# Performance work log

Hardware: AMD Instinct MI355X
Metric: run time of the kernel (lower is better)

Reference implementation:

```python
import jax, jax.numpy as jnp
import numpy as np

B, N, K, L, H = 8, 2048, 16, 4, 8
CONV = (64, 64, 128, 256)
W_DIM, N_CODES, E_DIM, P_DIM, FF = 512, 8, 64, 256, 512


def act(x):
    return jax.nn.leaky_relu(x, 0.2)


def ln(x, g, b, eps=1e-5):
    m = jnp.mean(x, -1, keepdims=True)
    v = jnp.mean((x - m) ** 2, -1, keepdims=True)
    return g * (x - m) / jnp.sqrt(v + eps) + b


# per-batch neighbor gather: f [C,N], i [N,K] -> [C,N,K]
gather_nb = jax.vmap(lambda f, i: f[:, i])


def knn_idx(y):  # y [B,3,N] -> [B,N,K]
    xx = jnp.sum(y * y, axis=1)
    inner = jnp.einsum('bcn,bcm->bnm', y, y)
    dist = 2.0 * inner - xx[:, :, None] - xx[:, None, :]  # negative sq dist
    return jax.lax.top_k(dist, K)[1]


def mha(q, kv, Wq, bq, Wk, bk, Wv, bv, Wo, bo):
    Bq, S, D = q.shape
    Sk = kv.shape[1]
    dh = D // H
    qh = (q @ Wq.T + bq).reshape(Bq, S, H, dh)
    kh = (kv @ Wk.T + bk).reshape(Bq, Sk, H, dh)
    vh = (kv @ Wv.T + bv).reshape(Bq, Sk, H, dh)
    a = jax.nn.softmax(jnp.einsum('bqhd,bkhd->bhqk', qh, kh) * (1.0 / np.sqrt(dh)))
    o = jnp.einsum('bhqk,bkhd->bqhd', a, vh).reshape(Bq, S, D)
    return o @ Wo.T + bo


def setup_inputs() -> dict:
    key = jax.random.key(0)
    ks = iter(jax.random.split(key, 48))
    nrm = lambda shape: jax.random.normal(next(ks), shape, jnp.float32) * 0.02
    d = {
        'x': jax.random.normal(next(ks), (B, N, 3), jnp.float32),
        'W_ec': nrm((CONV[0], 6)), 'b_ec': jnp.zeros((CONV[0],), jnp.float32),
        'Wc1': nrm((CONV[1], CONV[0])), 'bc1': jnp.zeros((CONV[1],), jnp.float32),
        'Wc2': nrm((CONV[2], CONV[1])), 'bc2': jnp.zeros((CONV[2],), jnp.float32),
        'Wc3': nrm((CONV[3], CONV[2])), 'bc3': jnp.zeros((CONV[3],), jnp.float32),
        'Wf': nrm((W_DIM, sum(CONV))), 'bf': jnp.zeros((W_DIM,), jnp.float32),
        'Wpc': nrm((P_DIM, E_DIM)), 'bpc': jnp.zeros((P_DIM,), jnp.float32),
        'Wpi': nrm((P_DIM, 3)), 'bpi': jnp.zeros((P_DIM,), jnp.float32),
        'Wq': nrm((L, 2, P_DIM, P_DIM)), 'bq': jnp.zeros((L, 2, P_DIM), jnp.float32),
        'Wk': nrm((L, 2, P_DIM, P_DIM)), 'bk': jnp.zeros((L, 2, P_DIM), jnp.float32),
        'Wv': nrm((L, 2, P_DIM, P_DIM)), 'bv': jnp.zeros((L, 2, P_DIM), jnp.float32),
        'Wo': nrm((L, 2, P_DIM, P_DIM)), 'bo': jnp.zeros((L, 2, P_DIM), jnp.float32),
        'ln1g': jnp.ones((L, P_DIM), jnp.float32), 'ln1b': jnp.zeros((L, P_DIM), jnp.float32),
        'ln2g': jnp.ones((L, P_DIM), jnp.float32), 'ln2b': jnp.zeros((L, P_DIM), jnp.float32),
        'Wff1': nrm((L, FF, P_DIM)), 'bff1': jnp.zeros((L, FF), jnp.float32),
        'Wff2': nrm((L, P_DIM, FF)), 'bff2': jnp.zeros((L, P_DIM), jnp.float32),
        'ln3g': jnp.ones((L, P_DIM), jnp.float32), 'ln3b': jnp.zeros((L, P_DIM), jnp.float32),
        'lnfg': jnp.ones((P_DIM,), jnp.float32), 'lnfb': jnp.zeros((P_DIM,), jnp.float32),
        'Wcm': nrm((E_DIM, P_DIM)), 'bcm': jnp.zeros((E_DIM,), jnp.float32),
    }
    return d


def reference(x, W_ec, b_ec, Wc1, bc1, Wc2, bc2, Wc3, bc3, Wf, bf, Wpc, bpc, Wpi, bpi,
              Wq, bq, Wk, bk, Wv, bv, Wo, bo, ln1g, ln1b, ln2g, ln2b,
              Wff1, bff1, Wff2, bff2, ln3g, ln3b, lnfg, lnfb, Wcm, bcm):
    y = jnp.transpose(x, (0, 2, 1))                      # [B,3,N]
    idx = knn_idx(y)                                     # [B,N,K]
    nb = gather_nb(y, idx)                               # [B,3,N,K]
    feats = jnp.concatenate([nb - y[..., None], jnp.broadcast_to(y[..., None], nb.shape)], axis=1)
    h = act(jnp.einsum('oc,bcnk->bonk', W_ec, feats) + b_ec[:, None, None])
    h = h.max(axis=3)                                    # [B,64,N]
    xs = [h]
    for Wl, bl in ((Wc1, bc1), (Wc2, bc2), (Wc3, bc3)):
        h = gather_nb(h, idx).max(axis=3)                # graph max pooling
        h = act(jnp.einsum('oc,bcn->bon', Wl, h) + bl[:, None])
        xs.append(h)
    h = jnp.concatenate(xs, axis=1)                      # [B,512,N]
    h = jnp.einsum('oc,bcn->bon', Wf, h) + bf[:, None]
    xm = h.max(axis=2)                                   # [B,512]
    q = act(xm.reshape(B, N_CODES, E_DIM) @ Wpc.T + bpc) # [B,8,256]
    mem = act(x @ Wpi.T + bpi)                           # [B,N,256]
    for l in range(L):
        q = ln(q + mha(q, q, Wq[l, 0], bq[l, 0], Wk[l, 0], bk[l, 0], Wv[l, 0], bv[l, 0], Wo[l, 0], bo[l, 0]), ln1g[l], ln1b[l])
        q = ln(q + mha(q, mem, Wq[l, 1], bq[l, 1], Wk[l, 1], bk[l, 1], Wv[l, 1], bv[l, 1], Wo[l, 1], bo[l, 1]), ln2g[l], ln2b[l])
        q = ln(q + (act(q @ Wff1[l].T + bff1[l]) @ Wff2[l].T + bff2[l]), ln3g[l], ln3b[l])
    q = ln(q, lnfg, lnfb)
    out = q @ Wcm.T + bcm                                # [B,8,64]
    return out.reshape(B, W_DIM)
```

## Files before the change

### kernel.cpp

```cpp
#include <hip/hip_runtime.h>
#include <math.h>

#define BN 8
#define NP 2048
#define KNN 16
#define NL 4
#define NH 8

typedef __attribute__((ext_vector_type(8))) short bf16x8;
typedef __attribute__((ext_vector_type(4))) float f32x4;

__device__ __forceinline__ unsigned short f2bf(float f) {
    unsigned u = __float_as_uint(f);
    unsigned r = (u + 0x7FFFu + ((u >> 16) & 1u)) >> 16;
    return (unsigned short)r;
}
__device__ __forceinline__ float bf2f(unsigned short s) {
    return __uint_as_float(((unsigned)s) << 16);
}
__device__ __forceinline__ unsigned fmono(float f) {
    unsigned u = __float_as_uint(f);
    return (u & 0x80000000u) ? ~u : (u | 0x80000000u);
}
__device__ __forceinline__ float funmono(unsigned k) {
    return (k & 0x80000000u) ? __uint_as_float(k ^ 0x80000000u) : __uint_as_float(~k);
}

__device__ __forceinline__ float gemv_dot(const unsigned short* __restrict__ wrow, const float* sm, int K8) {
    const uint4* w8 = (const uint4*)wrow;
    const float4* r4 = (const float4*)sm;
    float acc = 0.f;
    #pragma unroll 16
    for (int c = 0; c < K8; ++c) {
        uint4 wv = w8[c];
        float4 a0 = r4[c * 2], a1 = r4[c * 2 + 1];
        acc += a0.x * __uint_as_float(wv.x << 16);
        acc += a0.y * __uint_as_float(wv.x & 0xFFFF0000u);
        acc += a0.z * __uint_as_float(wv.y << 16);
        acc += a0.w * __uint_as_float(wv.y & 0xFFFF0000u);
        acc += a1.x * __uint_as_float(wv.z << 16);
        acc += a1.y * __uint_as_float(wv.z & 0xFFFF0000u);
        acc += a1.z * __uint_as_float(wv.w << 16);
        acc += a1.w * __uint_as_float(wv.w & 0xFFFF0000u);
    }
    return acc;
}

__device__ __forceinline__ unsigned long long shflx_u64(unsigned long long v, int j) {
    int lo = __shfl_xor((int)(unsigned)(v & 0xFFFFFFFFull), j);
    int hi = __shfl_xor((int)(unsigned)(v >> 32), j);
    return ((unsigned long long)(unsigned)hi << 32) | (unsigned)lo;
}

__device__ __forceinline__ unsigned sort64_u32(unsigned v, int lane) {
    #pragma unroll
    for (int k = 2; k <= 64; k <<= 1) {
        #pragma unroll
        for (int j = k >> 1; j > 0; j >>= 1) {
            unsigned o = (unsigned)__shfl_xor((int)v, j);
            bool up = ((lane & k) == 0);
            bool lower = ((lane & j) == 0);
            unsigned mn = v < o ? v : o;
            unsigned mx = v < o ? o : v;
            v = (up == lower) ? mn : mx;
        }
    }
    return v;
}

__device__ __forceinline__ unsigned long long sort64_u64(unsigned long long v, int lane) {
    #pragma unroll
    for (int k = 2; k <= 64; k <<= 1) {
        #pragma unroll
        for (int j = k >> 1; j > 0; j >>= 1) {
            unsigned long long o = shflx_u64(v, j);
            bool up = ((lane & k) == 0);
            bool lower = ((lane & j) == 0);
            unsigned long long mn = v < o ? v : o;
            unsigned long long mx = v < o ? o : v;
            v = (up == lower) ? mn : mx;
        }
    }
    return v;
}

__global__ __launch_bounds__(256) void knn_kernel(const float* __restrict__ x, int* __restrict__ idxout) {
    __shared__ unsigned long long cand[4][64];
    int tid = threadIdx.x;
    int wv = tid >> 6, lane = tid & 63;
    int p = blockIdx.x * 4 + wv;
    int b = p >> 11, n = p & 2047;
    const float* xb = x + (size_t)b * NP * 3;
    float cx = xb[n * 3 + 0], cy = xb[n * 3 + 1], cz = xb[n * 3 + 2];
    float xn = cx * cx + cy * cy + cz * cz;
    unsigned key[32];
    unsigned lmax = 0u;
    #pragma unroll
    for (int t = 0; t < 32; ++t) {
        int m = (t << 6) | lane;
        float mx = xb[m * 3 + 0], my = xb[m * 3 + 1], mz = xb[m * 3 + 2];
        float xxm = mx * mx + my * my + mz * mz;
        float inner = cx * mx + cy * my + cz * mz;
        float dd = 2.0f * inner - xn - xxm;
        unsigned u = __float_as_uint(dd);
        u = (u & 0x80000000u) ? ~u : (u | 0x80000000u);
        key[t] = u;
        lmax = lmax > u ? lmax : u;
    }
    unsigned sorted = sort64_u32(lmax, lane);
    unsigned S = (unsigned)__shfl((int)sorted, 48);
    int c = 0;
    #pragma unroll
    for (int t = 0; t < 32; ++t) c += (key[t] >= S) ? 1 : 0;
    int inc = c;
    #pragma unroll
    for (int d = 1; d < 64; d <<= 1) {
        int tsh = __shfl_up(inc, d);
        if (lane >= d) inc += tsh;
    }
    int C = __shfl(inc, 63);
    int* op = idxout + (size_t)p * KNN;
    if (C <= 64) {
        int off = inc - c;
        #pragma unroll
        for (int t = 0; t < 32; ++t) {
            if (key[t] >= S) {
                int m = (t << 6) | lane;
                cand[wv][off++] = ((unsigned long long)key[t] << 16) | (unsigned)(2047 - m);
            }
        }
        asm volatile("s_waitcnt lgkmcnt(0)" ::: "memory");
        unsigned long long ck = (lane < C) ? cand[wv][lane] : 0ull;
        ck = sort64_u64(ck, lane);
        if (lane >= 48) op[63 - lane] = 2047 - (int)(unsigned)(ck & 0xFFFFull);
    } else {
        unsigned taken = 0u;
        for (int r = 0; r < KNN; ++r) {
            unsigned long long best = 0ull;
            #pragma unroll
            for (int t = 0; t < 32; ++t) {
                if (!((taken >> t) & 1u)) {
                    int m = (t << 6) | lane;
                    unsigned long long ck = ((unsigned long long)key[t] << 16) | (unsigned)(2047 - m);
                    if (ck > best) best = ck;
                }
            }
            #pragma unroll
            for (int d = 1; d < 64; d <<= 1) {
                unsigned long long o = shflx_u64(best, d);
                if (o > best) best = o;
            }
            int m = 2047 - (int)(unsigned)(best & 0xFFFFull);
            if (lane == 0) op[r] = m;
            if ((m & 63) == lane) taken |= 1u << (m >> 6);
        }
    }
}

__global__ __launch_bounds__(256) void edge_conv_kernel(const float* __restrict__ x, const int* __restrict__ idx,
                                                        const float* __restrict__ Wec, const float* __restrict__ bec,
                                                        unsigned short* __restrict__ hcatT) {
    int tid = threadIdx.x;
    int g = tid >> 6, o = tid & 63;
    int p = blockIdx.x * 4 + g;
    int b = p >> 11;
    __shared__ float nb[4][KNN][3];
    __shared__ float ctr[4][3];
    if (o < KNN) {
        int j = idx[(size_t)p * KNN + o];
        const float* xp = x + ((size_t)b * NP + j) * 3;
        nb[g][o][0] = xp[0]; nb[g][o][1] = xp[1]; nb[g][o][2] = xp[2];
    }
    if (o >= KNN && o < KNN + 3) ctr[g][o - KNN] = x[(size_t)p * 3 + (o - KNN)];
    __syncthreads();
    float w0 = Wec[o * 6 + 0], w1 = Wec[o * 6 + 1], w2 = Wec[o * 6 + 2];
    float w3 = Wec[o * 6 + 3], w4 = Wec[o * 6 + 4], w5 = Wec[o * 6 + 5];
    float c0 = ctr[g][0], c1 = ctr[g][1], c2 = ctr[g][2];
    float base = bec[o] + w3 * c0 + w4 * c1 + w5 * c2;
    float m = -3.4e38f;
    #pragma unroll
    for (int k = 0; k < KNN; ++k) {
        float v = base + w0 * (nb[g][k][0] - c0) + w1 * (nb[g][k][1] - c1) + w2 * (nb[g][k][2] - c2);
        v = v > 0.f ? v : 0.2f * v;
        m = fmaxf(m, v);
    }
    hcatT[(size_t)p * 512 + o] = f2bf(m);
}

__global__ __launch_bounds__(256) void pool_bf16_kernel(const unsigned short* __restrict__ src, int s_coff,
                                                        const int* __restrict__ idx,
                                                        unsigned short* __restrict__ dst, int C) {
    int tid = threadIdx.x, wv = tid >> 6, lane = tid & 63;
    int p = blockIdx.x * 4 + wv;
    int b = p >> 11;
    const int* ip = idx + (size_t)p * KNN;
    const unsigned short* sb = src + (size_t)b * NP * 512 + s_coff;
    for (int c0 = 0; c0 < C; c0 += 64) {
        int ch = c0 + lane;
        float m = -3.4e38f;
        #pragma unroll
        for (int k = 0; k < KNN; ++k) {
            int j = ip[k];
            m = fmaxf(m, bf2f(sb[(size_t)j * 512 + ch]));
        }
        dst[(size_t)p * C + ch] = f2bf(m);
    }
}

__global__ __launch_bounds__(256) void mfma_conv64_kernel(const unsigned short* __restrict__ A,
                                                          const unsigned short* __restrict__ W,
                                                          const float* __restrict__ bias,
                                                          unsigned short* __restrict__ hcatT, int coff) {
    __shared__ unsigned short As[128][72];
    __shared__ unsigned short Bs[64][72];
    int m0 = blockIdx.x * 128, b = blockIdx.z;
    int tid = threadIdx.x;
    int lane = tid & 63, wave = tid >> 6;
    int wr = wave >> 1, wc = wave & 1;
    int quad = lane >> 4, l16 = lane & 15;
    {
        int r = tid >> 1, s = (tid & 1) * 32;
        const unsigned short* ap = A + (size_t)b * NP * 64 + (size_t)(m0 + r) * 64 + s;
        uint4 v0 = *(const uint4*)(ap);
        uint4 v1 = *(const uint4*)(ap + 8);
        uint4 v2 = *(const uint4*)(ap + 16);
        uint4 v3 = *(const uint4*)(ap + 24);
        *(uint4*)&As[r][s] = v0; *(uint4*)&As[r][s + 8] = v1;
        *(uint4*)&As[r][s + 16] = v2; *(uint4*)&As[r][s + 24] = v3;
    }
    {
        int r = tid >> 2, s = (tid & 3) * 16;
        const unsigned short* wp = W + r * 64 + s;
        *(uint4*)&Bs[r][s] = *(const uint4*)wp;
        *(uint4*)&Bs[r][s + 8] = *(const uint4*)(wp + 8);
    }
    __syncthreads();
    f32x4 acc[4][2] = {};
    #pragma unroll
    for (int k0 = 0; k0 < 64; k0 += 32) {
        bf16x8 af[4], bfv[2];
        #pragma unroll
        for (int i = 0; i < 4; ++i) af[i] = *(const bf16x8*)&As[wr * 64 + i * 16 + l16][k0 + quad * 8];
        #pragma unroll
        for (int j = 0; j < 2; ++j) bfv[j] = *(const bf16x8*)&Bs[wc * 32 + j * 16 + l16][k0 + quad * 8];
        #pragma unroll
        for (int i = 0; i < 4; ++i)
            #pragma unroll
            for (int j = 0; j < 2; ++j)
                acc[i][j] = __builtin_amdgcn_mfma_f32_16x16x32_bf16(af[i], bfv[j], acc[i][j], 0, 0, 0);
    }
    #pragma unroll
    for (int i = 0; i < 4; ++i) {
        #pragma unroll
        for (int r = 0; r < 4; ++r) {
            int pt = m0 + wr * 64 + i * 16 + quad * 4 + r;
            #pragma unroll
            for (int j = 0; j < 2; ++j) {
                int ch = wc * 32 + j * 16 + l16;
                float v = acc[i][j][r] + bias[ch];
                v = v > 0.f ? v : 0.2f * v;
                hcatT[((size_t)b * NP + pt) * 512 + coff + ch] = f2bf(v);
            }
        }
    }
}

__global__ __launch_bounds__(256) void wcast_kernel(const float* __restrict__ Wf, const float* __restrict__ Wc3,
                                                    const float* __restrict__ Wk, const float* __restrict__ Wv,
                                                    const float* __restrict__ bk, const float* __restrict__ bv,
                                                    const float* __restrict__ Wc1, const float* __restrict__ Wc2,
                                                    const float* __restrict__ Wq, const float* __restrict__ Wo,
                                                    const float* __restrict__ Wff1, const float* __restrict__ Wff2,
                                                    unsigned short* __restrict__ WfB, unsigned short* __restrict__ Wc3B,
                                                    unsigned short* __restrict__ WkvB, float* __restrict__ bkv,
                                                    unsigned short* __restrict__ Wc1B, unsigned short* __restrict__ Wc2B,
                                                    unsigned short* __restrict__ WtB, unsigned short* __restrict__ Wff1B,
                                                    unsigned short* __restrict__ Wff2B,
                                                    unsigned* __restrict__ xmk) {
    int id = blockIdx.x * 256 + threadIdx.x;
    if (id < 262144) { WfB[id] = f2bf(Wf[id]); return; }
    int j = id - 262144;
    if (j < 32768) { Wc3B[j] = f2bf(Wc3[j]); return; }
    j -= 32768;
    if (j < 524288) {
        int l = j >> 17, r = j & 131071;
        float v = (r < 65536) ? Wk[(size_t)(l * 2 + 1) * 65536 + r]
                              : Wv[(size_t)(l * 2 + 1) * 65536 + (r - 65536)];
        WkvB[j] = f2bf(v);
        return;
    }
    j -= 524288;
    if (j < 2048) {
        int l = j >> 9, r = j & 511;
        bkv[j] = (r < 256) ? bk[(l * 2 + 1) * 256 + r] : bv[(l * 2 + 1) * 256 + (r - 256)];
        return;
    }
    j -= 2048;
    if (j < 4096) { Wc1B[j] = f2bf(Wc1[j]); return; }
    j -= 4096;
    if (j < 8192) { Wc2B[j] = f2bf(Wc2[j]); return; }
    j -= 8192;
    if (j < 4096) { xmk[j] = 0u; return; }
    j -= 4096;
    if (j < 1572864) {
        int l = j / 393216;
        int r = j - l * 393216;
        int m = r >> 16, c = r & 65535;
        float v;
        if (m == 0)      v = Wq[(size_t)(l * 2 + 0) * 65536 + c];
        else if (m == 1) v = Wk[(size_t)(l * 2 + 0) * 65536 + c];
        else if (m == 2) v = Wv[(size_t)(l * 2 + 0) * 65536 + c];
        else if (m == 3) v = Wo[(size_t)(l * 2 + 0) * 65536 + c];
        else if (m == 4) v = Wq[(size_t)(l * 2 + 1) * 65536 + c];
        else             v = Wo[(size_t)(l * 2 + 1) * 65536 + c];
        WtB[j] = f2bf(v);
        return;
    }
    j -= 1572864;
    if (j < 524288) { Wff1B[j] = f2bf(Wff1[j]); return; }
    j -= 524288;
    if (j < 524288) { Wff2B[j] = f2bf(Wff2[j]); return; }
}

__global__ __launch_bounds__(256) void mfma_gemm_kernel(const unsigned short* __restrict__ A, size_t a_bstride,
                                                        const unsigned short* __restrict__ B, size_t b_bstride,
                                                        const float* __restrict__ bias, int bias_per_m,
                                                        void* __restrict__ C, size_t c_bstride, int c_rstride,
                                                        int K, int act, int out_bf16,
                                                        unsigned* __restrict__ xmk, int domax) {
    __shared__ unsigned short As[128][40];
    __shared__ unsigned short Bs[128][40];
    int m0 = blockIdx.x * 128, n0 = blockIdx.y * 128, b = blockIdx.z;
    int tid = threadIdx.x;
    int lane = tid & 63, wave = tid >> 6;
    int wr = wave >> 1, wc = wave & 1;
    int quad = lane >> 4, l16 = lane & 15;
    int r0 = tid >> 2, kc0 = (tid & 3) * 8;
    f32x4 acc[4][4] = {};
    const unsigned short* Ab = A + (size_t)b * a_bstride;
    const unsigned short* Bb = B + (size_t)b * b_bstride;
    for (int k0 = 0; k0 < K; k0 += 32) {
        uint4 a0 = *(const uint4*)(Ab + (size_t)(m0 + r0) * K + k0 + kc0);
        uint4 a1 = *(const uint4*)(Ab + (size_t)(m0 + r0 + 64) * K + k0 + kc0);
        uint4 b0 = *(const uint4*)(Bb + (size_t)(n0 + r0) * K + k0 + kc0);
        uint4 b1 = *(const uint4*)(Bb + (size_t)(n0 + r0 + 64) * K + k0 + kc0);
        __syncthreads();
        *(uint4*)&As[r0][kc0] = a0;
        *(uint4*)&As[r0 + 64][kc0] = a1;
        *(uint4*)&Bs[r0][kc0] = b0;
        *(uint4*)&Bs[r0 + 64][kc0] = b1;
        __syncthreads();
        bf16x8 af[4], bfv[4];
        #pragma unroll
        for (int i = 0; i < 4; ++i) af[i] = *(const bf16x8*)&As[wr * 64 + i * 16 + l16][quad * 8];
        #pragma unroll
        for (int j = 0; j < 4; ++j) bfv[j] = *(const bf16x8*)&Bs[wc * 64 + j * 16 + l16][quad * 8];
        #pragma unroll
        for (int i = 0; i < 4; ++i)
            #pragma unroll
            for (int j = 0; j < 4; ++j)
                acc[i][j] = __builtin_amdgcn_mfma_f32_16x16x32_bf16(af[i], bfv[j], acc[i][j], 0, 0, 0);
    }
    if (domax) {
        #pragma unroll
        for (int i = 0; i < 4; ++i) {
            #pragma unroll
            for (int r = 0; r < 4; ++r) {
                int m = m0 + wr * 64 + i * 16 + quad * 4 + r;
                float v = fmaxf(fmaxf(acc[i][0][r], acc[i][1][r]), fmaxf(acc[i][2][r], acc[i][3][r]));
                v += bias[m];
                #pragma unroll
                for (int off = 1; off <= 8; off <<= 1) v = fmaxf(v, __shfl_xor(v, off));
                if (l16 == 0) atomicMax(&xmk[(size_t)b * 512 + m], fmono(v));
            }
        }
        return;
    }
    #pragma unroll
    for (int i = 0; i < 4; ++i) {
        #pragma unroll
        for (int r = 0; r < 4; ++r) {
            int m = m0 + wr * 64 + i * 16 + quad * 4 + r;
            float bm = bias_per_m ? bias[m] : 0.f;
            #pragma unroll
            for (int j = 0; j < 4; ++j) {
                int n = n0 + wc * 64 + j * 16 + l16;
                float v = acc[i][j][r] + (bias_per_m ? bm : bias[n]);
                if (act) v = v > 0.f ? v : 0.2f * v;
                size_t off = (size_t)b * c_bstride + (size_t)m * c_rstride + n;
                if (out_bf16) ((unsigned short*)C)[off] = f2bf(v);
                else          ((float*)C)[off] = v;
            }
        }
    }
}

__global__ __launch_bounds__(256) void mfma_kv_all_kernel(const unsigned short* __restrict__ A,
                                                          const unsigned short* __restrict__ W,
                                                          const float* __restrict__ bkv,
                                                          unsigned short* __restrict__ KVall) {
    __shared__ unsigned short As[128][40];
    __shared__ unsigned short Bs[128][40];
    int m0 = blockIdx.x * 128;
    int nb = blockIdx.y & 3, l = blockIdx.y >> 2;
    int n0 = nb * 128;
    int b = blockIdx.z;
    int tid = threadIdx.x;
    int lane = tid & 63, wave = tid >> 6;
    int wr = wave >> 1, wc = wave & 1;
    int quad = lane >> 4, l16 = lane & 15;
    int r0 = tid >> 2, kc0 = (tid & 3) * 8;
    f32x4 acc[4][4] = {};
    const unsigned short* Ab = A + (size_t)b * NP * 256;
    const unsigned short* Bb = W + (size_t)l * 131072;
    const float* bias = bkv + l * 512;
    for (int k0 = 0; k0 < 256; k0 += 32) {
        uint4 a0 = *(const uint4*)(Ab + (size_t)(m0 + r0) * 256 + k0 + kc0);
        uint4 a1 = *(const uint4*)(Ab + (size_t)(m0 + r0 + 64) * 256 + k0 + kc0);
        uint4 b0 = *(const uint4*)(Bb + (size_t)(n0 + r0) * 256 + k0 + kc0);
        uint4 b1 = *(const uint4*)(Bb + (size_t)(n0 + r0 + 64) * 256 + k0 + kc0);
        __syncthreads();
        *(uint4*)&As[r0][kc0] = a0;
        *(uint4*)&As[r0 + 64][kc0] = a1;
        *(uint4*)&Bs[r0][kc0] = b0;
        *(uint4*)&Bs[r0 + 64][kc0] = b1;
        __syncthreads();
        bf16x8 af[4], bfv[4];
        #pragma unroll
        for (int i = 0; i < 4; ++i) af[i] = *(const bf16x8*)&As[wr * 64 + i * 16 + l16][quad * 8];
        #pragma unroll
        for (int j = 0; j < 4; ++j) bfv[j] = *(const bf16x8*)&Bs[wc * 64 + j * 16 + l16][quad * 8];
        #pragma unroll
        for (int i = 0; i < 4; ++i)
            #pragma unroll
            for (int j = 0; j < 4; ++j)
                acc[i][j] = __builtin_amdgcn_mfma_f32_16x16x32_bf16(af[i], bfv[j], acc[i][j], 0, 0, 0);
    }
    unsigned short* Cb = KVall + ((size_t)l * BN + b) * NP * 512;
    #pragma unroll
    for (int i = 0; i < 4; ++i) {
        #pragma unroll
        for (int r = 0; r < 4; ++r) {
            int m = m0 + wr * 64 + i * 16 + quad * 4 + r;
            #pragma unroll
            for (int j = 0; j < 4; ++j) {
                int n = n0 + wc * 64 + j * 16 + l16;
                Cb[(size_t)m * 512 + n] = f2bf(acc[i][j][r] + bias[n]);
            }
        }
    }
}

__global__ __launch_bounds__(256) void pc_kernel(const unsigned* __restrict__ xmk, const float* __restrict__ Wpc,
                                                 const float* __restrict__ bpc, float* __restrict__ q) {
    int id = blockIdx.x * 256 + threadIdx.x;
    int p = id & 255;
    int rowi = id >> 8;
    int b = rowi >> 3, i = rowi & 7;
    const unsigned* xr = xmk + b * 512 + i * 64;
    const float* w = Wpc + (size_t)p * 64;
    float acc = bpc[p];
    #pragma unroll
    for (int e = 0; e < 64; ++e) acc += funmono(xr[e]) * w[e];
    q[id] = acc > 0.f ? acc : 0.2f * acc;
}

__global__ __launch_bounds__(256) void mem_kernel(const float* __restrict__ x, const float* __restrict__ Wpi,
                                                  const float* __restrict__ bpi, unsigned short* __restrict__ memB) {
    size_t id = (size_t)blockIdx.x * 256 + threadIdx.x;
    int p = (int)(id & 255);
    size_t pt = id >> 8;
    float x0 = x[pt * 3 + 0], x1 = x[pt * 3 + 1], x2 = x[pt * 3 + 2];
    float v = bpi[p] + x0 * Wpi[p * 3 + 0] + x1 * Wpi[p * 3 + 1] + x2 * Wpi[p * 3 + 2];
    v = v > 0.f ? v : 0.2f * v;
    memB[id] = f2bf(v);
}

__global__ __launch_bounds__(256) void qkv_proj_kernel(const float* __restrict__ in,
                                                       const unsigned short* __restrict__ WB,
                                                       const float* __restrict__ bq0, const float* __restrict__ bk0,
                                                       const float* __restrict__ bv0,
                                                       float* __restrict__ Qs, float* __restrict__ Ks,
                                                       float* __restrict__ Vs) {
    int which = blockIdx.y;
    const unsigned short* W = WB + (size_t)which * 65536;
    const float* bb = (which == 0) ? bq0 : (which == 1) ? bk0 : bv0;
    float* out = (which == 0) ? Qs : (which == 1) ? Ks : Vs;
    __shared__ __align__(16) float r[256];
    int row = blockIdx.x, tid = threadIdx.x;
    r[tid] = in[(size_t)row * 256 + tid];
    __syncthreads();
    float acc = bb[tid] + gemv_dot(W + (size_t)tid * 256, r, 32);
    out[(size_t)row * 256 + tid] = acc;
}

__global__ __launch_bounds__(256) void attn_ln_kernel(const float* __restrict__ Qs, const float* __restrict__ Ks,
                                                      const float* __restrict__ Vs,
                                                      const unsigned short* __restrict__ WoB,
                                                      const float* __restrict__ bo, const float* __restrict__ res,
                                                      const float* __restrict__ g, const float* __restrict__ bt,
                                                      const unsigned short* __restrict__ Wq1B,
                                                      const float* __restrict__ bq1,
                                                      float* __restrict__ out, float* __restrict__ Qc) {
    int row = blockIdx.x, tid = threadIdx.x;
    int b = row >> 3;
    __shared__ float Kl[2048], Vl[2048], qr[256];
    __shared__ float sc[64];
    __shared__ __align__(16) float r[256];
    __shared__ __align__(16) float aout[256];
    __shared__ float red[256];
    for (int t = tid; t < 2048; t += 256) {
        Kl[t] = Ks[(size_t)b * 2048 + t];
        Vl[t] = Vs[(size_t)b * 2048 + t];
    }
    qr[tid] = Qs[(size_t)row * 256 + tid];
    __syncthreads();
    const float scale = 0.17677669529663687f;
    if (tid < 64) {
        int h = tid >> 3, k = tid & 7;
        float dot = 0.f;
        #pragma unroll
        for (int d = 0; d < 32; ++d) dot += qr[h * 32 + d] * Kl[k * 256 + h * 32 + d];
        sc[tid] = dot * scale;
    }
    __syncthreads();
    if (tid < 8) {
        float* p = sc + tid * 8;
        float m = -3.4e38f;
        #pragma unroll
        for (int k = 0; k < 8; ++k) m = fmaxf(m, p[k]);
        float s = 0.f;
        #pragma unroll
        for (int k = 0; k < 8; ++k) { p[k] = __expf(p[k] - m); s += p[k]; }
        float inv = 1.f / s;
        #pragma unroll
        for (int k = 0; k < 8; ++k) p[k] *= inv;
    }
    __syncthreads();
    {
        int h = tid >> 5;
        float acc = 0.f;
        #pragma unroll
        for (int k = 0; k < 8; ++k) acc += sc[h * 8 + k] * Vl[k * 256 + tid];
        r[tid] = acc;
    }
    __syncthreads();
    float acc = bo[tid] + gemv_dot(WoB + (size_t)tid * 256, r, 32);
    float v = res[(size_t)row * 256 + tid] + acc;
    red[tid] = v; __syncthreads();
    for (int s = 128; s; s >>= 1) { if (tid < s) red[tid] += red[tid + s]; __syncthreads(); }
    float mean = red[0] * (1.0f / 256.0f);
    __syncthreads();
    float dv = v - mean;
    red[tid] = dv * dv; __syncthreads();
    for (int s = 128; s; s >>= 1) { if (tid < s) red[tid] += red[tid + s]; __syncthreads(); }
    float var = red[0] * (1.0f / 256.0f);
    float oln = g[tid] * dv * rsqrtf(var + 1e-5f) + bt[tid];
    out[(size_t)row * 256 + tid] = oln;
    aout[tid] = oln;
    __syncthreads();
    {
        float qacc = bq1[tid] + gemv_dot(Wq1B + (size_t)tid * 256, aout, 32);
        Qc[(size_t)row * 256 + tid] = qacc;
    }
}

__global__ __launch_bounds__(256) void ca_part_kernel(const float* __restrict__ Qc,
                                                      const unsigned short* __restrict__ KVl,
                                                      float* __restrict__ part) {
    int kb = blockIdx.x, h = blockIdx.y, b = blockIdx.z;
    int tid = threadIdx.x;
    __shared__ float q[8][32];
    __shared__ __align__(16) float S[8][128];
    __shared__ float om[8][8][32];
    const float scale = 0.17677669529663687f;
    {
        int i = tid >> 5, d = tid & 31;
        q[i][d] = Qc[(size_t)(b * 8 + i) * 256 + h * 32 + d];
    }
    __syncthreads();
    {
        int kk = tid & 127, half = tid >> 7;
        int k = kb * 128 + kk;
        const unsigned short* kp = KVl + ((size_t)b * NP + k) * 512 + h * 32;
        float kd[32];
        #pragma unroll
        for (int u = 0; u < 4; ++u) {
            uint4 raw = *(const uint4*)(kp + u * 8);
            unsigned w0 = raw.x, w1 = raw.y, w2 = raw.z, w3 = raw.w;
            kd[u * 8 + 0] = __uint_as_float(w0 << 16); kd[u * 8 + 1] = __uint_as_float(w0 & 0xFFFF0000u);
            kd[u * 8 + 2] = __uint_as_float(w1 << 16); kd[u * 8 + 3] = __uint_as_float(w1 & 0xFFFF0000u);
            kd[u * 8 + 4] = __uint_as_float(w2 << 16); kd[u * 8 + 5] = __uint_as_float(w2 & 0xFFFF0000u);
            kd[u * 8 + 6] = __uint_as_float(w3 << 16); kd[u * 8 + 7] = __uint_as_float(w3 & 0xFFFF0000u);
        }
        #pragma unroll
        for (int i = 0; i < 4; ++i) {
            int ri = half * 4 + i;
            float dot = 0.f;
            #pragma unroll
            for (int d = 0; d < 32; ++d) dot += q[ri][d] * kd[d];
            S[ri][kk] = dot * scale;
        }
    }
    __syncthreads();
    float* pout = part + (((size_t)(b * NH + h)) * 16 + kb) * 288;
    {
        int i = tid >> 5, l32 = tid & 31;
        float m = -3.4e38f;
        #pragma unroll
        for (int t = 0; t < 4; ++t) m = fmaxf(m, S[i][l32 + t * 32]);
        #pragma unroll
        for (int off = 16; off; off >>= 1) m = fmaxf(m, __shfl_xor(m, off));
        float s = 0.f;
        #pragma unroll
        for (int t = 0; t < 4; ++t) {
            float e = __expf(S[i][l32 + t * 32] - m);
            S[i][l32 + t * 32] = e;
            s += e;
        }
        #pragma unroll
        for (int off = 16; off; off >>= 1) s += __shfl_xor(s, off);
        if (l32 == 0) { pout[i] = m; pout[8 + i] = s; }
    }
    __syncthreads();
    {
        int d = tid & 31, grp = tid >> 5;
        const unsigned short* Vb = KVl + ((size_t)b * NP + kb * 128) * 512 + 256 + h * 32 + d;
        float acc[8] = {};
        #pragma unroll 4
        for (int t = 0; t < 16; ++t) {
            int kk = grp * 16 + t;
            float v = bf2f(Vb[(size_t)kk * 512]);
            #pragma unroll
            for (int i = 0; i < 8; ++i) acc[i] += S[i][kk] * v;
        }
        #pragma unroll
        for (int i = 0; i < 8; ++i) om[grp][i][d] = acc[i];
    }
    __syncthreads();
    {
        int i = tid >> 5, d = tid & 31;
        float sum = 0.f;
        #pragma unroll
        for (int g = 0; g < 8; ++g) sum += om[g][i][d];
        pout[16 + i * 32 + d] = sum;
    }
}

__global__ __launch_bounds__(256) void combine_ff_kernel(const float* __restrict__ part,
                                                         const unsigned short* __restrict__ WoB,
                                                         const float* __restrict__ bo, const float* __restrict__ res,
                                                         const float* __restrict__ g2, const float* __restrict__ b2t,
                                                         const unsigned short* __restrict__ W1B,
                                                         const float* __restrict__ b1,
                                                         const unsigned short* __restrict__ W2B,
                                                         const float* __restrict__ b2,
                                                         const float* __restrict__ g3, const float* __restrict__ b3t,
                                                         float* __restrict__ out,
                                                         int is_last, const float* __restrict__ lnfg,
                                                         const float* __restrict__ lnfb, const float* __restrict__ Wcm,
                                                         const float* __restrict__ bcm, float* __restrict__ finout) {
    int row = blockIdx.x, tid = threadIdx.x;
    int b = row >> 3, i = row & 7;
    __shared__ __align__(16) float r[256];
    __shared__ __align__(16) float a[256];
    __shared__ __align__(16) float hbuf[512];
    __shared__ float red[256];
    {
        int h = tid >> 5, d = tid & 31;
        const float* pb = part + (size_t)(b * NH + h) * 16 * 288;
        float M = -3.4e38f;
        #pragma unroll
        for (int kb = 0; kb < 16; ++kb) M = fmaxf(M, pb[kb * 288 + i]);
        float L = 0.f, O = 0.f;
        #pragma unroll
        for (int kb = 0; kb < 16; ++kb) {
            float w = __expf(pb[kb * 288 + i] - M);
            L += pb[kb * 288 + 8 + i] * w;
            O += pb[kb * 288 + 16 + i * 32 + d] * w;
        }
        r[tid] = O / L;
    }
    __syncthreads();
    {
        float acc = bo[tid] + gemv_dot(WoB + (size_t)tid * 256, r, 32);
        float v = res[(size_t)row * 256 + tid] + acc;
        red[tid] = v; __syncthreads();
        for (int s = 128; s; s >>= 1) { if (tid < s) red[tid] += red[tid + s]; __syncthreads(); }
        float mean = red[0] * (1.0f / 256.0f);
        __syncthreads();
        float dv = v - mean;
        red[tid] = dv * dv; __syncthreads();
        for (int s = 128; s; s >>= 1) { if (tid < s) red[tid] += red[tid + s]; __syncthreads(); }
        float var = red[0] * (1.0f / 256.0f);
        a[tid] = g2[tid] * dv * rsqrtf(var + 1e-5f) + b2t[tid];
    }
    __syncthreads();
    {
        #pragma unroll
        for (int half = 0; half < 2; ++half) {
            int o = tid + half * 256;
            float acc = b1[o] + gemv_dot(W1B + (size_t)o * 256, a, 32);
            hbuf[o] = acc > 0.f ? acc : 0.2f * acc;
        }
    }
    __syncthreads();
    float tln;
    {
        float acc = b2[tid] + gemv_dot(W2B + (size_t)tid * 512, hbuf, 64);
        float v = a[tid] + acc;
        red[tid] = v; __syncthreads();
        for (int s = 128; s; s >>= 1) { if (tid < s) red[tid] += red[tid + s]; __syncthreads(); }
        float mean = red[0] * (1.0f / 256.0f);
        __syncthreads();
        float dv = v - mean;
        red[tid] = dv * dv; __syncthreads();
        for (int s = 128; s; s >>= 1) { if (tid < s) red[tid] += red[tid + s]; __syncthreads(); }
        float var = red[0] * (1.0f / 256.0f);
        tln = g3[tid] * dv * rsqrtf(var + 1e-5f) + b3t[tid];
    }
    if (!is_last) {
        out[(size_t)row * 256 + tid] = tln;
        return;
    }
    __syncthreads();
    red[tid] = tln; __syncthreads();
    for (int s = 128; s; s >>= 1) { if (tid < s) red[tid] += red[tid + s]; __syncthreads(); }
    float mean = red[0] * (1.0f / 256.0f);
    __syncthreads();
    float dv = tln - mean;
    red[tid] = dv * dv; __syncthreads();
    for (int s = 128; s; s >>= 1) { if (tid < s) red[tid] += red[tid + s]; __syncthreads(); }
    float var = red[0] * (1.0f / 256.0f);
    a[tid] = lnfg[tid] * dv * rsqrtf(var + 1e-5f) + lnfb[tid];
    __syncthreads();
    if (tid < 64) {
        const float4* w4 = (const float4*)(Wcm + (size_t)tid * 256);
        const float4* a4 = (const float4*)a;
        float acc = bcm[tid];
        #pragma unroll 8
        for (int c = 0; c < 64; ++c) {
            float4 av = a4[c], wv = w4[c];
            acc += av.x * wv.x + av.y * wv.y + av.z * wv.z + av.w * wv.w;
        }
        finout[(size_t)b * 512 + i * 64 + tid] = acc;
    }
}

extern "C" void kernel_launch(void* const* d_in, const int* in_sizes, int n_in,
                              void* d_out, int out_size, void* d_ws, size_t ws_size,
                              hipStream_t stream) {
    const float* x    = (const float*)d_in[0];
    const float* Wec  = (const float*)d_in[1];
    const float* bec  = (const float*)d_in[2];
    const float* Wc1  = (const float*)d_in[3];
    const float* bc1  = (const float*)d_in[4];
    const float* Wc2  = (const float*)d_in[5];
    const float* bc2  = (const float*)d_in[6];
    const float* Wc3  = (const float*)d_in[7];
    const float* bc3  = (const float*)d_in[8];
    const float* Wf   = (const float*)d_in[9];
    const float* bf   = (const float*)d_in[10];
    const float* Wpc  = (const float*)d_in[11];
    const float* bpc  = (const float*)d_in[12];
    const float* Wpi  = (const float*)d_in[13];
    const float* bpi  = (const float*)d_in[14];
    const float* Wq   = (const float*)d_in[15];
    const float* bq   = (const float*)d_in[16];
    const float* Wk   = (const float*)d_in[17];
    const float* bk   = (const float*)d_in[18];
    const float* Wv   = (const float*)d_in[19];
    const float* bv   = (const float*)d_in[20];
    const float* Wo   = (const float*)d_in[21];
    const float* bo   = (const float*)d_in[22];
    const float* ln1g = (const float*)d_in[23];
    const float* ln1b = (const float*)d_in[24];
    const float* ln2g = (const float*)d_in[25];
    const float* ln2b = (const float*)d_in[26];
    const float* Wff1 = (const float*)d_in[27];
    const float* bff1 = (const float*)d_in[28];
    const float* Wff2 = (const float*)d_in[29];
    const float* bff2 = (const float*)d_in[30];
    const float* ln3g = (const float*)d_in[31];
    const float* ln3b = (const float*)d_in[32];
    const float* lnfg = (const float*)d_in[33];
    const float* lnfb = (const float*)d_in[34];
    const float* Wcm  = (const float*)d_in[35];
    const float* bcm  = (const float*)d_in[36];
    float* out = (float*)d_out;

    float* ws = (float*)d_ws;
    size_t off = 0;
    auto alloc = [&](size_t n) { float* p = ws + off; off += (n + 3) & ~(size_t)3; return p; };
    int*            idx   = (int*)alloc((size_t)BN * NP * KNN);
    unsigned short* hcatT = (unsigned short*)alloc((size_t)BN * NP * 512 / 2);
    unsigned short* poolT = (unsigned short*)alloc((size_t)BN * NP * 128 / 2);
    unsigned short* WfB   = (unsigned short*)alloc(262144 / 2);
    unsigned short* Wc1B  = (unsigned short*)alloc(4096 / 2);
    unsigned short* Wc2B  = (unsigned short*)alloc(8192 / 2);
    unsigned short* Wc3B  = (unsigned short*)alloc(32768 / 2);
    unsigned short* WkvB  = (unsigned short*)alloc(524288 / 2);
    float*          bkv   = alloc(2048);
    unsigned short* memB  = (unsigned short*)alloc((size_t)BN * NP * 256 / 2);
    unsigned short* KVall = (unsigned short*)alloc((size_t)NL * BN * NP * 512 / 2);
    unsigned*       xmk   = (unsigned*)alloc((size_t)BN * 512);
    unsigned short* WtB   = (unsigned short*)alloc(1572864 / 2);
    unsigned short* Wff1B = (unsigned short*)alloc(524288 / 2);
    unsigned short* Wff2B = (unsigned short*)alloc(524288 / 2);
    float*          qa    = alloc((size_t)BN * 8 * 256);
    float*          qb    = alloc((size_t)BN * 8 * 256);
    float*          Qs    = alloc((size_t)BN * 8 * 256);
    float*          Ks    = alloc((size_t)BN * 8 * 256);
    float*          Vs    = alloc((size_t)BN * 8 * 256);
    float*          Qc    = alloc((size_t)BN * 8 * 256);
    float*          part  = alloc((size_t)BN * NH * 16 * 288);

    wcast_kernel<<<13512, 256, 0, stream>>>(Wf, Wc3, Wk, Wv, bk, bv, Wc1, Wc2, Wq, Wo, Wff1, Wff2,
                                            WfB, Wc3B, WkvB, bkv, Wc1B, Wc2B, WtB, Wff1B, Wff2B, xmk);

    knn_kernel<<<BN * NP / 4, 256, 0, stream>>>(x, idx);
    edge_conv_kernel<<<BN * NP / 4, 256, 0, stream>>>(x, idx, Wec, bec, hcatT);

    pool_bf16_kernel<<<BN * NP / 4, 256, 0, stream>>>(hcatT, 0, idx, poolT, 64);
    mfma_conv64_kernel<<<dim3(NP / 128, 1, BN), 256, 0, stream>>>(poolT, Wc1B, bc1, hcatT, 64);
    pool_bf16_kernel<<<BN * NP / 4, 256, 0, stream>>>(hcatT, 64, idx, poolT, 64);
    mfma_gemm_kernel<<<dim3(NP / 128, 1, BN), 256, 0, stream>>>(poolT, (size_t)NP * 64, Wc2B, 0,
                                                                bc2, 0, (void*)(hcatT + 128), (size_t)NP * 512, 512,
                                                                64, 1, 1, nullptr, 0);
    pool_bf16_kernel<<<BN * NP / 4, 256, 0, stream>>>(hcatT, 128, idx, poolT, 128);
    mfma_gemm_kernel<<<dim3(NP / 128, 2, BN), 256, 0, stream>>>(poolT, (size_t)NP * 128, Wc3B, 0,
                                                                bc3, 0, (void*)(hcatT + 256), (size_t)NP * 512, 512,
                                                                128, 1, 1, nullptr, 0);
    mfma_gemm_kernel<<<dim3(4, NP / 128, BN), 256, 0, stream>>>(WfB, 0, hcatT, (size_t)NP * 512,
                                                                bf, 1, nullptr, 0, 0,
                                                                512, 0, 0, xmk, 1);
    pc_kernel<<<BN * 8, 256, 0, stream>>>(xmk, Wpc, bpc, qa);
    mem_kernel<<<BN * NP, 256, 0, stream>>>(x, Wpi, bpi, memB);
    mfma_kv_all_kernel<<<dim3(NP / 128, 4 * NL, BN), 256, 0, stream>>>(memB, WkvB, bkv, KVall);

    float* qcur = qa; float* qnxt = qb;
    for (int l = 0; l < NL; ++l) {
        const unsigned short* Wl = WtB + (size_t)l * 393216;
        const float* bq0 = bq + (l * 2 + 0) * 256;
        const float* bk0 = bk + (l * 2 + 0) * 256;
        const float* bv0 = bv + (l * 2 + 0) * 256;
        const float* bo0 = bo + (l * 2 + 0) * 256;
        const float* bq1 = bq + (l * 2 + 1) * 256;
        const float* bo1 = bo + (l * 2 + 1) * 256;
        int last = (l == NL - 1);

        qkv_proj_kernel<<<dim3(BN * 8, 3), 256, 0, stream>>>(qcur, Wl, bq0, bk0, bv0, Qs, Ks, Vs);
        attn_ln_kernel<<<BN * 8, 256, 0, stream>>>(Qs, Ks, Vs, Wl + 3 * 65536, bo0, qcur,
                                                   ln1g + l * 256, ln1b + l * 256, Wl + 4 * 65536, bq1, qnxt, Qc);
        ca_part_kernel<<<dim3(16, NH, BN), 256, 0, stream>>>(Qc, KVall + (size_t)l * BN * NP * 512, part);
        combine_ff_kernel<<<BN * 8, 256, 0, stream>>>(part, Wl + 5 * 65536, bo1, qnxt,
                                                      ln2g + l * 256, ln2b + l * 256,
                                                      Wff1B + (size_t)l * 131072, bff1 + l * 512,
                                                      Wff2B + (size_t)l * 131072, bff2 + l * 256,
                                                      ln3g + l * 256, ln3b + l * 256, qcur,
                                                      last, lnfg, lnfb, Wcm, bcm, out);
    }

    (void)in_sizes; (void)n_in; (void)out_size; (void)ws_size; (void)qnxt;
}
```

Measured before the change: 561.6 us.

## Fuse self-attention QKV projection into preceding pc and combine_ff kernels

Removes the separate qkv_proj kernel. The QKV projection for layer 0 now runs at the end of pc_kernel, and for each later layer at the end of the previous layer's combine_ff_kernel. This cuts one launch per layer, but each of those blocks now serially does three GEMVs where there used to be 3x as many blocks. The attention scores and softmax in attn_ln are also parallelised over more threads using wave shuffles instead of a few serial threads.

```diff
diff --git a/kernel.cpp b/kernel.cpp
--- a/kernel.cpp
+++ b/kernel.cpp
@@ -452,17 +452,28 @@
 }
 
 __global__ __launch_bounds__(256) void pc_kernel(const unsigned* __restrict__ xmk, const float* __restrict__ Wpc,
-                                                 const float* __restrict__ bpc, float* __restrict__ q) {
-    int id = blockIdx.x * 256 + threadIdx.x;
-    int p = id & 255;
-    int rowi = id >> 8;
-    int b = rowi >> 3, i = rowi & 7;
+                                                 const float* __restrict__ bpc,
+                                                 const unsigned short* __restrict__ Wqkv,
+                                                 const float* __restrict__ bq0, const float* __restrict__ bk0,
+                                                 const float* __restrict__ bv0,
+                                                 float* __restrict__ q, float* __restrict__ Qs,
+                                                 float* __restrict__ Ks, float* __restrict__ Vs) {
+    int row = blockIdx.x, tid = threadIdx.x;
+    int id = row * 256 + tid;
+    int b = row >> 3, i = row & 7;
     const unsigned* xr = xmk + b * 512 + i * 64;
-    const float* w = Wpc + (size_t)p * 64;
-    float acc = bpc[p];
+    const float* w = Wpc + (size_t)tid * 64;
+    float acc = bpc[tid];
     #pragma unroll
     for (int e = 0; e < 64; ++e) acc += funmono(xr[e]) * w[e];
-    q[id] = acc > 0.f ? acc : 0.2f * acc;
+    float qv = acc > 0.f ? acc : 0.2f * acc;
+    q[id] = qv;
+    __shared__ __align__(16) float a[256];
+    a[tid] = qv;
+    __syncthreads();
+    Qs[id] = bq0[tid] + gemv_dot(Wqkv + (size_t)tid * 256, a, 32);
+    Ks[id] = bk0[tid] + gemv_dot(Wqkv + 65536 + (size_t)tid * 256, a, 32);
+    Vs[id] = bv0[tid] + gemv_dot(Wqkv + 131072 + (size_t)tid * 256, a, 32);
 }
 
 __global__ __launch_bounds__(256) void mem_kernel(const float* __restrict__ x, const float* __restrict__ Wpi,
@@ -474,24 +485,6 @@
     float v = bpi[p] + x0 * Wpi[p * 3 + 0] + x1 * Wpi[p * 3 + 1] + x2 * Wpi[p * 3 + 2];
     v = v > 0.f ? v : 0.2f * v;
     memB[id] = f2bf(v);
-}
-
-__global__ __launch_bounds__(256) void qkv_proj_kernel(const float* __restrict__ in,
-                                                       const unsigned short* __restrict__ WB,
-                                                       const float* __restrict__ bq0, const float* __restrict__ bk0,
-                                                       const float* __restrict__ bv0,
-                                                       float* __restrict__ Qs, float* __restrict__ Ks,
-                                                       float* __restrict__ Vs) {
-    int which = blockIdx.y;
-    const unsigned short* W = WB + (size_t)which * 65536;
-    const float* bb = (which == 0) ? bq0 : (which == 1) ? bk0 : bv0;
-    float* out = (which == 0) ? Qs : (which == 1) ? Ks : Vs;
-    __shared__ __align__(16) float r[256];
-    int row = blockIdx.x, tid = threadIdx.x;
-    r[tid] = in[(size_t)row * 256 + tid];
-    __syncthreads();
-    float acc = bb[tid] + gemv_dot(W + (size_t)tid * 256, r, 32);
-    out[(size_t)row * 256 + tid] = acc;
 }
 
 __global__ __launch_bounds__(256) void attn_ln_kernel(const float* __restrict__ Qs, const float* __restrict__ Ks,
@@ -516,25 +509,32 @@
     qr[tid] = Qs[(size_t)row * 256 + tid];
     __syncthreads();
     const float scale = 0.17677669529663687f;
+    {
+        int pair = tid >> 2, part = tid & 3;
+        int h = pair >> 3, k = pair & 7;
+        float dot = 0.f;
+        #pragma unroll
+        for (int d0 = 0; d0 < 8; ++d0) {
+            int d = part * 8 + d0;
+            dot += qr[h * 32 + d] * Kl[k * 256 + h * 32 + d];
+        }
+        dot += __shfl_xor(dot, 1);
+        dot += __shfl_xor(dot, 2);
+        if (part == 0) sc[pair] = dot * scale;
+    }
+    __syncthreads();
     if (tid < 64) {
-        int h = tid >> 3, k = tid & 7;
-        float dot = 0.f;
-        #pragma unroll
-        for (int d = 0; d < 32; ++d) dot += qr[h * 32 + d] * Kl[k * 256 + h * 32 + d];
-        sc[tid] = dot * scale;
-    }
-    __syncthreads();
-    if (tid < 8) {
-        float* p = sc + tid * 8;
-        float m = -3.4e38f;
-        #pragma unroll
-        for (int k = 0; k < 8; ++k) m = fmaxf(m, p[k]);
-        float s = 0.f;
-        #pragma unroll
-        for (int k = 0; k < 8; ++k) { p[k] = __expf(p[k] - m); s += p[k]; }
-        float inv = 1.f / s;
-        #pragma unroll
-        for (int k = 0; k < 8; ++k) p[k] *= inv;
+        int k = tid & 7;
+        float v = sc[tid];
+        float m = v;
+        #pragma unroll
+        for (int off = 1; off < 8; off <<= 1) m = fmaxf(m, __shfl_xor(m, off));
+        float e = __expf(v - m);
+        float s = e;
+        #pragma unroll
+        for (int off = 1; off < 8; off <<= 1) s += __shfl_xor(s, off);
+        sc[tid] = e / s;
+        (void)k;
     }
     __syncthreads();
     {
@@ -659,7 +659,12 @@
                                                          float* __restrict__ out,
                                                          int is_last, const float* __restrict__ lnfg,
                                                          const float* __restrict__ lnfb, const float* __restrict__ Wcm,
-                                                         const float* __restrict__ bcm, float* __restrict__ finout) {
+                                                         const float* __restrict__ bcm, float* __restrict__ finout,
+                                                         const unsigned short* __restrict__ Wqkvn,
+                                                         const float* __restrict__ bqn, const float* __restrict__ bkn,
+                                                         const float* __restrict__ bvn,
+                                                         float* __restrict__ Qs, float* __restrict__ Ks,
+                                                         float* __restrict__ Vs) {
     int row = blockIdx.x, tid = threadIdx.x;
     int b = row >> 3, i = row & 7;
     __shared__ __align__(16) float r[256];
@@ -721,6 +726,12 @@
     }
     if (!is_last) {
         out[(size_t)row * 256 + tid] = tln;
+        r[tid] = tln;
+        __syncthreads();
+        size_t id = (size_t)row * 256 + tid;
+        Qs[id] = bqn[tid] + gemv_dot(Wqkvn + (size_t)tid * 256, r, 32);
+        Ks[id] = bkn[tid] + gemv_dot(Wqkvn + 65536 + (size_t)tid * 256, r, 32);
+        Vs[id] = bvn[tid] + gemv_dot(Wqkvn + 131072 + (size_t)tid * 256, r, 32);
         return;
     }
     __syncthreads();
@@ -834,32 +845,31 @@
     mfma_gemm_kernel<<<dim3(4, NP / 128, BN), 256, 0, stream>>>(WfB, 0, hcatT, (size_t)NP * 512,
                                                                 bf, 1, nullptr, 0, 0,
                                                                 512, 0, 0, xmk, 1);
-    pc_kernel<<<BN * 8, 256, 0, stream>>>(xmk, Wpc, bpc, qa);
+    pc_kernel<<<BN * 8, 256, 0, stream>>>(xmk, Wpc, bpc, WtB, bq, bk, bv, qa, Qs, Ks, Vs);
     mem_kernel<<<BN * NP, 256, 0, stream>>>(x, Wpi, bpi, memB);
     mfma_kv_all_kernel<<<dim3(NP / 128, 4 * NL, BN), 256, 0, stream>>>(memB, WkvB, bkv, KVall);
 
-    float* qcur = qa; float* qnxt = qb;
     for (int l = 0; l < NL; ++l) {
         const unsigned short* Wl = WtB + (size_t)l * 393216;
-        const float* bq0 = bq + (l * 2 + 0) * 256;
-        const float* bk0 = bk + (l * 2 + 0) * 256;
-        const float* bv0 = bv + (l * 2 + 0) * 256;
         const float* bo0 = bo + (l * 2 + 0) * 256;
         const float* bq1 = bq + (l * 2 + 1) * 256;
         const float* bo1 = bo + (l * 2 + 1) * 256;
         int last = (l == NL - 1);
 
-        qkv_proj_kernel<<<dim3(BN * 8, 3), 256, 0, stream>>>(qcur, Wl, bq0, bk0, bv0, Qs, Ks, Vs);
-        attn_ln_kernel<<<BN * 8, 256, 0, stream>>>(Qs, Ks, Vs, Wl + 3 * 65536, bo0, qcur,
-                                                   ln1g + l * 256, ln1b + l * 256, Wl + 4 * 65536, bq1, qnxt, Qc);
+        attn_ln_kernel<<<BN * 8, 256, 0, stream>>>(Qs, Ks, Vs, Wl + 3 * 65536, bo0, qa,
+                                                   ln1g + l * 256, ln1b + l * 256, Wl + 4 * 65536, bq1, qb, Qc);
         ca_part_kernel<<<dim3(16, NH, BN), 256, 0, stream>>>(Qc, KVall + (size_t)l * BN * NP * 512, part);
-        combine_ff_kernel<<<BN * 8, 256, 0, stream>>>(part, Wl + 5 * 65536, bo1, qnxt,
+        combine_ff_kernel<<<BN * 8, 256, 0, stream>>>(part, Wl + 5 * 65536, bo1, qb,
                                                       ln2g + l * 256, ln2b + l * 256,
                                                       Wff1B + (size_t)l * 131072, bff1 + l * 512,
                                                       Wff2B + (size_t)l * 131072, bff2 + l * 256,
-                                                      ln3g + l * 256, ln3b + l * 256, qcur,
-                                                      last, lnfg, lnfb, Wcm, bcm, out);
-    }
-
-    (void)in_sizes; (void)n_in; (void)out_size; (void)ws_size; (void)qnxt;
-}
+                                                      ln3g + l * 256, ln3b + l * 256, qa,
+                                                      last, lnfg, lnfb, Wcm, bcm, out,
+                                                      last ? nullptr : WtB + (size_t)(l + 1) * 393216,
+                                                      bq + ((l + 1) * 2) * 256, bk + ((l + 1) * 2) * 256,
+                                                      bv + ((l + 1) * 2) * 256,
+                                                      Qs, Ks, Vs);
+    }
+
+    (void)in_sizes; (void)n_in; (void)out_size; (void)ws_size;
+}
```

Measured after the change: 591.7 us. 5.4% more time.
